# Performance work log

Hardware: AMD Instinct MI355X
Metric: run time of the kernel (lower is better)

Reference implementation:

```python
import jax, jax.numpy as jnp
import numpy as np

N_OBS = 6000
N_X = 6000
D_FEAT = 16
N_DOM = 3


def _block_ranges(n, d):
    b = np.linspace(0, n, d + 1).astype(np.int32)
    return jnp.asarray(np.stack([b[:-1], b[1:]], axis=1))  # [d,2] (start,end)


def setup_inputs() -> dict:
    key = jax.random.key(0)
    ks = jax.random.split(key, 6)
    xobs = jax.random.normal(ks[0], (N_OBS, D_FEAT), jnp.float32)
    x = jax.random.normal(ks[1], (N_X, D_FEAT), jnp.float32)
    w = jnp.round(jax.random.uniform(ks[2], (N_X, 1), jnp.float32))  # binary treatment
    alpha0 = jax.random.uniform(ks[3], (N_OBS, 1), jnp.float32)
    alpha1 = jax.random.uniform(ks[4], (N_OBS, 1), jnp.float32)
    n_pairs = N_DOM * (N_DOM - 1) // 2
    transfer_factor_logit = 0.1 * jax.random.normal(ks[5], (n_pairs,), jnp.float32)
    raw_lengthscale = jnp.zeros((), jnp.float32)  # gpytorch raw param; softplus(0)~0.693
    return {
        "xobs": xobs, "x": x, "w": w,
        "alpha0": alpha0, "alpha1": alpha1,
        "transfer_factor_logit": transfer_factor_logit,
        "raw_lengthscale": raw_lengthscale,
        "domain_ranges_obs": _block_ranges(N_OBS, N_DOM),
        "domain_ranges_x": _block_ranges(N_X, N_DOM),
    }


def _matern52(x1, x2, lengthscale):
    # gpytorch MaternKernel(nu=5/2): k(d)=(1+sqrt5*d+5/3*d^2)exp(-sqrt5*d), d=||x1-x2||/ls
    x1 = x1 / lengthscale
    x2 = x2 / lengthscale
    sq = (jnp.sum(x1 * x1, 1)[:, None] + jnp.sum(x2 * x2, 1)[None, :]
          - 2.0 * (x1 @ x2.T))
    d = jnp.sqrt(jnp.maximum(sq, 1e-12))
    s5d = jnp.sqrt(jnp.asarray(5.0, d.dtype)) * d
    return (1.0 + s5d + (5.0 / 3.0) * d * d) * jnp.exp(-s5d)


def _domain_ids(n, ranges):
    # contiguous sorted partition: id = #starts <= idx  - 1
    idx = jnp.arange(n)
    return jnp.sum(idx[:, None] >= ranges[None, :, 0], axis=1) - 1


def reference(xobs, x, w, alpha0, alpha1, transfer_factor_logit,
              raw_lengthscale, domain_ranges_obs, domain_ranges_x):
    ls = jax.nn.softplus(raw_lengthscale)
    M = _matern52(xobs, x, ls)                       # [N_obs, N_x]
    # pairwise transfer factor matrix F[di,dj]: 1 on diagonal, sigmoid(logit_n)
    # for pair n enumerated as (i<j) row-major, matching the original loop order
    tf = jax.nn.sigmoid(transfer_factor_logit)
    iu, ju = np.triu_indices(N_DOM, 1)
    F = jnp.ones((N_DOM, N_DOM), M.dtype).at[iu, ju].set(tf).at[ju, iu].set(tf)
    dom_o = _domain_ids(xobs.shape[0], domain_ranges_obs)   # [N_obs]
    dom_x = _domain_ids(x.shape[0], domain_ranges_x)        # [N_x]
    K = M * F[dom_o[:, None], dom_x[None, :]]               # fused transfer blend
    f0 = alpha0[:, 0] @ K                                   # [N_x]
    f1 = alpha1[:, 0] @ K
    wv = w.reshape(-1)
    return wv * f0 + (1.0 - wv) * f1
```

## Files before the change

### kernel.cpp

```cpp
#include <hip/hip_runtime.h>
#include <math.h>

typedef _Float16 f16x8 __attribute__((ext_vector_type(8)));
typedef float    f32x4 __attribute__((ext_vector_type(4)));

__global__ __launch_bounds__(256) void prep_split(
    const float* __restrict__ xobs, const float* __restrict__ x,
    const float* __restrict__ rawls,
    _Float16* __restrict__ ap,
    _Float16* __restrict__ bh,
    _Float16* __restrict__ bl,
    float* __restrict__ no2, float* __restrict__ nx2,
    int n_obs, int n_x)
{
    const int i = blockIdx.x * 256 + threadIdx.x;
    const float r  = rawls[0];
    const float ls = fmaxf(r, 0.f) + log1pf(__expf(-fabsf(r)));
    const float inv_ls2 = 1.f / (ls * ls);

    if (i < n_obs) {
        float s = 0.f;
        #pragma unroll
        for (int k = 0; k < 16; ++k) {
            const float v = xobs[(size_t)i * 16 + k];
            s = fmaf(v, v, s);
            const _Float16 h = (_Float16)v;
            ap[(size_t)i * 32 + k]      = h;
            ap[(size_t)i * 32 + 16 + k] = (_Float16)(v - (float)h);
        }
        no2[i] = s * inv_ls2;
    }
    if (i < n_x) {
        float s = 0.f;
        #pragma unroll
        for (int k = 0; k < 16; ++k) {
            const float v = x[(size_t)i * 16 + k];
            s = fmaf(v, v, s);
            const _Float16 h = (_Float16)v;
            bh[(size_t)i * 16 + k] = h;
            bl[(size_t)i * 16 + k] = (_Float16)(v - (float)h);
        }
        nx2[i] = s * inv_ls2;
    }
}

__global__ __launch_bounds__(256, 4) void matern_mfma(
    const _Float16* __restrict__ ap, const _Float16* __restrict__ bh,
    const _Float16* __restrict__ bl,
    const float* __restrict__ no2, const float* __restrict__ nx2,
    const float* __restrict__ alpha0, const float* __restrict__ alpha1,
    const float* __restrict__ tfl, const float* __restrict__ rawls,
    const int* __restrict__ rngo, const int* __restrict__ rngx,
    float* __restrict__ f01, int n_obs, int n_x, int ntiles_i, int tiles_per_chunk)
{
    const int wave = threadIdx.x >> 6;
    const int lane = threadIdx.x & 63;
    const int njt  = n_x >> 4;
    const int jt   = blockIdx.x * 4 + wave;
    if (jt >= njt) return;
    const int g16 = lane >> 4;
    const int l16 = lane & 15;
    const int j   = jt * 16 + l16;

    const f16x8 B1 = *(const f16x8*)(bh + (size_t)j * 16 + (g16 & 1) * 8);
    f16x8 B2 = f16x8{0, 0, 0, 0, 0, 0, 0, 0};
    if (g16 < 2) B2 = *(const f16x8*)(bl + (size_t)j * 16 + g16 * 8);

    const float r  = rawls[0];
    const float ls = fmaxf(r, 0.f) + log1pf(__expf(-fabsf(r)));
    const float inv_ls2 = 1.f / (ls * ls);
    const float c2  = -2.f * inv_ls2;
    const float nxj = nx2[j];

    const float t0 = 1.f / (1.f + __expf(-tfl[0]));
    const float t1 = 1.f / (1.f + __expf(-tfl[1]));
    const float t2 = 1.f / (1.f + __expf(-tfl[2]));
    const int dxj = (j >= rngx[2] ? 1 : 0) + (j >= rngx[4] ? 1 : 0);
    const float fdr0 = (dxj == 0) ? 1.f : ((dxj == 1) ? t0 : t1);
    const float fdr1 = (dxj == 0) ? t0  : ((dxj == 1) ? 1.f : t2);
    const float fdr2 = (dxj == 0) ? t1  : ((dxj == 1) ? t2  : 1.f);

    const float S5   = 2.2360679774997896f;
    const float C53  = 5.0f / 3.0f;
    const float NL2E = -1.4426950408889634f;

    float s0 = 0.f, s1 = 0.f;
    const int it0 = blockIdx.y * tiles_per_chunk;
    const int it1 = min(it0 + tiles_per_chunk, ntiles_i);

    for (int it = it0; it < it1; ++it) {
        const int ibase = it * 16;
        const f16x8 A1 = *(const f16x8*)(ap + (size_t)(ibase + l16) * 32 + g16 * 8);
        f32x4 acc = {0.f, 0.f, 0.f, 0.f};
        acc = __builtin_amdgcn_mfma_f32_16x16x32_f16(A1, B1, acc, 0, 0, 0);
        acc = __builtin_amdgcn_mfma_f32_16x16x32_f16(A1, B2, acc, 0, 0, 0);

        const int rbase = ibase + g16 * 4;
        const f32x4 nov = *(const f32x4*)(no2   + rbase);
        const f32x4 a0v = *(const f32x4*)(alpha0 + rbase);
        const f32x4 a1v = *(const f32x4*)(alpha1 + rbase);

        const int domi = (ibase >= rngo[2] ? 1 : 0) + (ibase >= rngo[4] ? 1 : 0);
        const float fd = (domi == 0) ? fdr0 : ((domi == 1) ? fdr1 : fdr2);

        #pragma unroll
        for (int rr = 0; rr < 4; ++rr) {
            float sq = fmaf(c2, acc[rr], nov[rr] + nxj);
            sq = fmaxf(sq, 1e-12f);
            const float rs   = __frsqrt_rn(sq);
            const float dd   = sq * rs;
            const float s5d  = S5 * dd;
            const float poly = fmaf(C53, sq, 1.f + s5d);
            const float e    = __builtin_amdgcn_exp2f(NL2E * s5d);
            const float m    = poly * e;
            s0 = fmaf(fd * a0v[rr], m, s0);
            s1 = fmaf(fd * a1v[rr], m, s1);
        }
    }

    s0 += __shfl_xor(s0, 16, 64);
    s0 += __shfl_xor(s0, 32, 64);
    s1 += __shfl_xor(s1, 16, 64);
    s1 += __shfl_xor(s1, 32, 64);
    if (g16 == 0) {
        atomicAdd(&f01[j], s0);
        atomicAdd(&f01[n_x + j], s1);
    }
}

__global__ void combine_out(const float* __restrict__ w,
                            const float* __restrict__ f01,
                            float* __restrict__ out, int n_x)
{
    const int j = blockIdx.x * 256 + threadIdx.x;
    if (j < n_x) {
        const float wv = w[j];
        out[j] = wv * f01[j] + (1.f - wv) * f01[n_x + j];
    }
}

extern "C" void kernel_launch(void* const* d_in, const int* in_sizes, int n_in,
                              void* d_out, int out_size, void* d_ws, size_t ws_size,
                              hipStream_t stream)
{
    const float* xobs = (const float*)d_in[0];
    const float* x    = (const float*)d_in[1];
    const float* w    = (const float*)d_in[2];
    const float* a0   = (const float*)d_in[3];
    const float* a1   = (const float*)d_in[4];
    const float* tfl  = (const float*)d_in[5];
    const float* rls  = (const float*)d_in[6];
    const int*   rngo = (const int*)d_in[7];
    const int*   rngx = (const int*)d_in[8];

    const int n_obs = in_sizes[0] / 16;
    const int n_x   = in_sizes[1] / 16;

    char* p = (char*)d_ws;
    auto take = [&](size_t bytes) { char* q = p; p += (bytes + 255) & ~(size_t)255; return q; };
    float*     f01 = (float*)    take(sizeof(float) * 2 * (size_t)n_x);
    _Float16*  ap  = (_Float16*) take(sizeof(_Float16) * 32 * (size_t)n_obs);
    _Float16*  bh  = (_Float16*) take(sizeof(_Float16) * 16 * (size_t)n_x);
    _Float16*  bl  = (_Float16*) take(sizeof(_Float16) * 16 * (size_t)n_x);
    float*     no2 = (float*)    take(sizeof(float) * (size_t)n_obs);
    float*     nx2 = (float*)    take(sizeof(float) * (size_t)n_x);

    (void)hipMemsetAsync(f01, 0, sizeof(float) * 2 * (size_t)n_x, stream);

    const int nmax = (n_obs > n_x) ? n_obs : n_x;
    prep_split<<<(nmax + 255) / 256, 256, 0, stream>>>(xobs, x, rls, ap, bh, bl,
                                                       no2, nx2, n_obs, n_x);

    const int njt = n_x / 16;
    const int ntiles_i = n_obs / 16;
    const int tiles_per_chunk = 15;
    const int gy = (ntiles_i + tiles_per_chunk - 1) / tiles_per_chunk;
    dim3 grid((njt + 3) / 4, gy);
    matern_mfma<<<grid, 256, 0, stream>>>(ap, bh, bl, no2, nx2, a0, a1, tfl, rls,
                                          rngo, rngx, f01, n_obs, n_x,
                                          ntiles_i, tiles_per_chunk);

    combine_out<<<(n_x + 255) / 256, 256, 0, stream>>>(w, f01, (float*)d_out, n_x);
}
```

Baseline: 101.9 us.

## Prescale norms by five, prefold transfer factors into alpha, unroll tile loop by two

Norms are stored scaled by 5/ls^2, so the inner loop works directly in units of 5*d^2. This drops the S5 multiply and the separate dd computation. The prep kernel builds three copies of alpha0 and alpha1, each pre-multiplied by the transfer factor for one x-domain, which removes the per-tile domain select and the factor multiply from the hot loop. The main loop now handles two i-tiles per iteration to overlap loads and MFMA latency, at the cost of more registers and a larger workspace. The clamp epsilon is adjusted to match the new scaling.

Result: no change. 101.6 us (-0.3%).

```diff
diff --git a/kernel.cpp b/kernel.cpp
--- a/kernel.cpp
+++ b/kernel.cpp
@@ -6,17 +6,20 @@
 
 __global__ __launch_bounds__(256) void prep_split(
     const float* __restrict__ xobs, const float* __restrict__ x,
-    const float* __restrict__ rawls,
+    const float* __restrict__ alpha0, const float* __restrict__ alpha1,
+    const float* __restrict__ tfl, const float* __restrict__ rawls,
+    const int* __restrict__ rngo,
     _Float16* __restrict__ ap,
     _Float16* __restrict__ bh,
     _Float16* __restrict__ bl,
-    float* __restrict__ no2, float* __restrict__ nx2,
+    float* __restrict__ no5, float* __restrict__ nx5,
+    float* __restrict__ a0f, float* __restrict__ a1f,
     int n_obs, int n_x)
 {
     const int i = blockIdx.x * 256 + threadIdx.x;
     const float r  = rawls[0];
     const float ls = fmaxf(r, 0.f) + log1pf(__expf(-fabsf(r)));
-    const float inv_ls2 = 1.f / (ls * ls);
+    const float s5_ls2 = 5.f / (ls * ls);
 
     if (i < n_obs) {
         float s = 0.f;
@@ -28,7 +31,22 @@
             ap[(size_t)i * 32 + k]      = h;
             ap[(size_t)i * 32 + 16 + k] = (_Float16)(v - (float)h);
         }
-        no2[i] = s * inv_ls2;
+        no5[i] = s * s5_ls2;
+
+        const float t0 = 1.f / (1.f + __expf(-tfl[0]));
+        const float t1 = 1.f / (1.f + __expf(-tfl[1]));
+        const float t2 = 1.f / (1.f + __expf(-tfl[2]));
+        const int dom = (i >= rngo[2] ? 1 : 0) + (i >= rngo[4] ? 1 : 0);
+        const float F0 = (dom == 0) ? 1.f : ((dom == 1) ? t0 : t1);
+        const float F1 = (dom == 0) ? t0  : ((dom == 1) ? 1.f : t2);
+        const float F2 = (dom == 0) ? t1  : ((dom == 1) ? t2  : 1.f);
+        const float av0 = alpha0[i], av1 = alpha1[i];
+        a0f[i]              = av0 * F0;
+        a0f[n_obs + i]      = av0 * F1;
+        a0f[2 * n_obs + i]  = av0 * F2;
+        a1f[i]              = av1 * F0;
+        a1f[n_obs + i]      = av1 * F1;
+        a1f[2 * n_obs + i]  = av1 * F2;
     }
     if (i < n_x) {
         float s = 0.f;
@@ -40,17 +58,16 @@
             bh[(size_t)i * 16 + k] = h;
             bl[(size_t)i * 16 + k] = (_Float16)(v - (float)h);
         }
-        nx2[i] = s * inv_ls2;
+        nx5[i] = s * s5_ls2;
     }
 }
 
 __global__ __launch_bounds__(256, 4) void matern_mfma(
     const _Float16* __restrict__ ap, const _Float16* __restrict__ bh,
     const _Float16* __restrict__ bl,
-    const float* __restrict__ no2, const float* __restrict__ nx2,
-    const float* __restrict__ alpha0, const float* __restrict__ alpha1,
-    const float* __restrict__ tfl, const float* __restrict__ rawls,
-    const int* __restrict__ rngo, const int* __restrict__ rngx,
+    const float* __restrict__ no5, const float* __restrict__ nx5,
+    const float* __restrict__ a0f, const float* __restrict__ a1f,
+    const float* __restrict__ rawls, const int* __restrict__ rngx,
     float* __restrict__ f01, int n_obs, int n_x, int ntiles_i, int tiles_per_chunk)
 {
     const int wave = threadIdx.x >> 6;
@@ -68,55 +85,70 @@
 
     const float r  = rawls[0];
     const float ls = fmaxf(r, 0.f) + log1pf(__expf(-fabsf(r)));
-    const float inv_ls2 = 1.f / (ls * ls);
-    const float c2  = -2.f * inv_ls2;
-    const float nxj = nx2[j];
-
-    const float t0 = 1.f / (1.f + __expf(-tfl[0]));
-    const float t1 = 1.f / (1.f + __expf(-tfl[1]));
-    const float t2 = 1.f / (1.f + __expf(-tfl[2]));
+    const float c2_5 = -10.f / (ls * ls);
+    const float nx5j = nx5[j];
+
     const int dxj = (j >= rngx[2] ? 1 : 0) + (j >= rngx[4] ? 1 : 0);
-    const float fdr0 = (dxj == 0) ? 1.f : ((dxj == 1) ? t0 : t1);
-    const float fdr1 = (dxj == 0) ? t0  : ((dxj == 1) ? 1.f : t2);
-    const float fdr2 = (dxj == 0) ? t1  : ((dxj == 1) ? t2  : 1.f);
-
-    const float S5   = 2.2360679774997896f;
-    const float C53  = 5.0f / 3.0f;
+    const float* __restrict__ a0p = a0f + (size_t)dxj * n_obs;
+    const float* __restrict__ a1p = a1f + (size_t)dxj * n_obs;
+
+    const float C13  = 1.f / 3.f;
     const float NL2E = -1.4426950408889634f;
 
     float s0 = 0.f, s1 = 0.f;
     const int it0 = blockIdx.y * tiles_per_chunk;
     const int it1 = min(it0 + tiles_per_chunk, ntiles_i);
 
-    for (int it = it0; it < it1; ++it) {
-        const int ibase = it * 16;
-        const f16x8 A1 = *(const f16x8*)(ap + (size_t)(ibase + l16) * 32 + g16 * 8);
-        f32x4 acc = {0.f, 0.f, 0.f, 0.f};
-        acc = __builtin_amdgcn_mfma_f32_16x16x32_f16(A1, B1, acc, 0, 0, 0);
-        acc = __builtin_amdgcn_mfma_f32_16x16x32_f16(A1, B2, acc, 0, 0, 0);
-
-        const int rbase = ibase + g16 * 4;
-        const f32x4 nov = *(const f32x4*)(no2   + rbase);
-        const f32x4 a0v = *(const f32x4*)(alpha0 + rbase);
-        const f32x4 a1v = *(const f32x4*)(alpha1 + rbase);
-
-        const int domi = (ibase >= rngo[2] ? 1 : 0) + (ibase >= rngo[4] ? 1 : 0);
-        const float fd = (domi == 0) ? fdr0 : ((domi == 1) ? fdr1 : fdr2);
-
-        #pragma unroll
-        for (int rr = 0; rr < 4; ++rr) {
-            float sq = fmaf(c2, acc[rr], nov[rr] + nxj);
-            sq = fmaxf(sq, 1e-12f);
-            const float rs   = __frsqrt_rn(sq);
-            const float dd   = sq * rs;
-            const float s5d  = S5 * dd;
-            const float poly = fmaf(C53, sq, 1.f + s5d);
-            const float e    = __builtin_amdgcn_exp2f(NL2E * s5d);
-            const float m    = poly * e;
-            s0 = fmaf(fd * a0v[rr], m, s0);
-            s1 = fmaf(fd * a1v[rr], m, s1);
+    #define TAIL4(ACC, NOV, A0V, A1V)                                        \
+        _Pragma("unroll")                                                    \
+        for (int rr = 0; rr < 4; ++rr) {                                     \
+            float u = fmaf(c2_5, (ACC)[rr], (NOV)[rr] + nx5j);               \
+            u = fmaxf(u, 1e-11f);                                            \
+            const float rs   = __frsqrt_rn(u);                               \
+            const float s5d  = u * rs;                          \
+            const float poly = fmaf(C13, u, 1.f + s5d);                      \
+            const float e    = __builtin_amdgcn_exp2f(NL2E * s5d);           \
+            const float m    = poly * e;                                     \
+            s0 = fmaf((A0V)[rr], m, s0);                                     \
+            s1 = fmaf((A1V)[rr], m, s1);                                     \
         }
-    }
+
+    int it = it0;
+    for (; it + 1 < it1; it += 2) {
+        const int ia = it * 16, ib = ia + 16;
+        const f16x8 Aa = *(const f16x8*)(ap + (size_t)(ia + l16) * 32 + g16 * 8);
+        const f16x8 Ab = *(const f16x8*)(ap + (size_t)(ib + l16) * 32 + g16 * 8);
+        const int ra = ia + g16 * 4, rb = ib + g16 * 4;
+        const f32x4 nova = *(const f32x4*)(no5 + ra);
+        const f32x4 novb = *(const f32x4*)(no5 + rb);
+        const f32x4 a0a  = *(const f32x4*)(a0p + ra);
+        const f32x4 a0b  = *(const f32x4*)(a0p + rb);
+        const f32x4 a1a  = *(const f32x4*)(a1p + ra);
+        const f32x4 a1b  = *(const f32x4*)(a1p + rb);
+
+        f32x4 acca = {0.f, 0.f, 0.f, 0.f};
+        acca = __builtin_amdgcn_mfma_f32_16x16x32_f16(Aa, B1, acca, 0, 0, 0);
+        acca = __builtin_amdgcn_mfma_f32_16x16x32_f16(Aa, B2, acca, 0, 0, 0);
+        f32x4 accb = {0.f, 0.f, 0.f, 0.f};
+        accb = __builtin_amdgcn_mfma_f32_16x16x32_f16(Ab, B1, accb, 0, 0, 0);
+        accb = __builtin_amdgcn_mfma_f32_16x16x32_f16(Ab, B2, accb, 0, 0, 0);
+
+        TAIL4(acca, nova, a0a, a1a)
+        TAIL4(accb, novb, a0b, a1b)
+    }
+    if (it < it1) {
+        const int ia = it * 16;
+        const f16x8 Aa = *(const f16x8*)(ap + (size_t)(ia + l16) * 32 + g16 * 8);
+        const int ra = ia + g16 * 4;
+        const f32x4 nova = *(const f32x4*)(no5 + ra);
+        const f32x4 a0a  = *(const f32x4*)(a0p + ra);
+        const f32x4 a1a  = *(const f32x4*)(a1p + ra);
+        f32x4 acca = {0.f, 0.f, 0.f, 0.f};
+        acca = __builtin_amdgcn_mfma_f32_16x16x32_f16(Aa, B1, acca, 0, 0, 0);
+        acca = __builtin_amdgcn_mfma_f32_16x16x32_f16(Aa, B2, acca, 0, 0, 0);
+        TAIL4(acca, nova, a0a, a1a)
+    }
+    #undef TAIL4
 
     s0 += __shfl_xor(s0, 16, 64);
     s0 += __shfl_xor(s0, 32, 64);
@@ -162,22 +194,24 @@
     _Float16*  ap  = (_Float16*) take(sizeof(_Float16) * 32 * (size_t)n_obs);
     _Float16*  bh  = (_Float16*) take(sizeof(_Float16) * 16 * (size_t)n_x);
     _Float16*  bl  = (_Float16*) take(sizeof(_Float16) * 16 * (size_t)n_x);
-    float*     no2 = (float*)    take(sizeof(float) * (size_t)n_obs);
-    float*     nx2 = (float*)    take(sizeof(float) * (size_t)n_x);
+    float*     no5 = (float*)    take(sizeof(float) * (size_t)n_obs);
+    float*     nx5 = (float*)    take(sizeof(float) * (size_t)n_x);
+    float*     a0f = (float*)    take(sizeof(float) * 3 * (size_t)n_obs);
+    float*     a1f = (float*)    take(sizeof(float) * 3 * (size_t)n_obs);
 
     (void)hipMemsetAsync(f01, 0, sizeof(float) * 2 * (size_t)n_x, stream);
 
     const int nmax = (n_obs > n_x) ? n_obs : n_x;
-    prep_split<<<(nmax + 255) / 256, 256, 0, stream>>>(xobs, x, rls, ap, bh, bl,
-                                                       no2, nx2, n_obs, n_x);
+    prep_split<<<(nmax + 255) / 256, 256, 0, stream>>>(
+        xobs, x, a0, a1, tfl, rls, rngo, ap, bh, bl, no5, nx5, a0f, a1f, n_obs, n_x);
 
     const int njt = n_x / 16;
     const int ntiles_i = n_obs / 16;
     const int tiles_per_chunk = 15;
     const int gy = (ntiles_i + tiles_per_chunk - 1) / tiles_per_chunk;
     dim3 grid((njt + 3) / 4, gy);
-    matern_mfma<<<grid, 256, 0, stream>>>(ap, bh, bl, no2, nx2, a0, a1, tfl, rls,
-                                          rngo, rngx, f01, n_obs, n_x,
+    matern_mfma<<<grid, 256, 0, stream>>>(ap, bh, bl, no5, nx5, a0f, a1f, rls,
+                                          rngx, f01, n_obs, n_x,
                                           ntiles_i, tiles_per_chunk);
 
     combine_out<<<(n_x + 255) / 256, 256, 0, stream>>>(w, f01, (float*)d_out, n_x);
```
